# Performance work log

Hardware: AMD Instinct MI355X
Metric: run time of the kernel (lower is better)

## Reference

```python
import jax, jax.numpy as jnp
import numpy as np

N, S = 65536, 2048        # dense points, sampled centres
D1, D2 = 64, 256          # skip-feature dim, centre-embedding dim
MLP = [256, 128]          # conv1x1 channel stack
BN_EPS = 1e-5             # flax BatchNorm default
INTERP_EPS = 1e-8


def setup_inputs() -> dict:
    key = jax.random.key(0)
    ks = jax.random.split(key, 6)
    inp = {
        "xyz1": jax.random.normal(ks[0], (3, N), jnp.float32),
        "xyz2": jax.random.normal(ks[1], (3, S), jnp.float32),
        "points1": jax.random.normal(ks[2], (D1, N), jnp.float32),
        "points2": jax.random.normal(ks[3], (D2, S), jnp.float32),
    }
    c_in = D1 + D2
    for i, c_out in enumerate(MLP):
        inp[f"w{i}"] = jax.random.normal(ks[4 + i], (c_in, c_out), jnp.float32) / np.float32(np.sqrt(c_in))
        inp[f"b{i}"] = jnp.zeros((c_out,), jnp.float32)
        inp[f"scale{i}"] = jnp.ones((c_out,), jnp.float32)
        inp[f"bias{i}"] = jnp.zeros((c_out,), jnp.float32)
        inp[f"mean{i}"] = jnp.zeros((c_out,), jnp.float32)   # BN running mean
        inp[f"var{i}"] = jnp.ones((c_out,), jnp.float32)     # BN running var
        c_in = c_out
    return inp


def reference(xyz1, xyz2, points1, points2,
              w0, b0, scale0, bias0, mean0, var0,
              w1, b1, scale1, bias1, mean1, var1):
    x1 = xyz1.T            # [N, 3]
    x2 = xyz2.T            # [S, 3]
    p2 = points2.T         # [S, D2]

    # squared pairwise distances [N, S]
    dists = (jnp.sum(x1 * x1, -1, keepdims=True)
             + jnp.sum(x2 * x2, -1)[None, :]
             - 2.0 * (x1 @ x2.T))

    # 3 nearest neighbours (smallest dist) per dense point
    neg_d3, idx = jax.lax.top_k(-dists, 3)      # [N, 3]
    d3 = -neg_d3
    recip = 1.0 / (d3 + INTERP_EPS)
    w = recip / jnp.sum(recip, axis=1, keepdims=True)   # [N, 3]

    # inverse-distance-weighted interpolation: [N, D2]
    interp = jnp.einsum('nkd,nk->nd', p2[idx], w)

    new = jnp.concatenate([points1.T, interp], axis=-1)  # [N, D1+D2]

    # conv1x1 (== dense) + BN (inference, running stats) + ReLU stack
    for W, b, s, bb, m, v in ((w0, b0, scale0, bias0, mean0, var0),
                              (w1, b1, scale1, bias1, mean1, var1)):
        y = new @ W + b
        y = (y - m) * (s / jnp.sqrt(v + BN_EPS)) + bb
        new = jax.nn.relu(y)

    return new.T           # [MLP[-1], N]
```

## Files before the change

kernel.cpp:

```cpp
#include <hip/hip_runtime.h>
#include <math.h>

#define NPTS 65536
#define NS   2048
#define C2   256
#define C3   128

#define WS_XYZ2P   0
#define WS_P2T     32768
#define WS_W0F     1081344
#define WS_W1F     1245184
#define WS_AB0     1310720
#define WS_AB1     1312768
#define WS_KIDX    1313792
#define WS_KW      2100224

typedef __attribute__((ext_vector_type(8))) short bf16x8;
typedef __attribute__((ext_vector_type(4))) float f32x4;

__device__ __forceinline__ unsigned short f2bf(float f) {
  unsigned u = __builtin_bit_cast(unsigned, f);
  u = (u + 0x7FFFu + ((u >> 16) & 1u)) >> 16;
  return (unsigned short)u;
}
__device__ __forceinline__ float bf2f(unsigned h) {
  return __builtin_bit_cast(float, h << 16);
}

__global__ __launch_bounds__(256) void pnfp_prep(
    const float* __restrict__ xyz2,
    const float* __restrict__ w0, const float* __restrict__ b0,
    const float* __restrict__ scale0, const float* __restrict__ bias0,
    const float* __restrict__ mean0, const float* __restrict__ var0,
    const float* __restrict__ w1, const float* __restrict__ b1,
    const float* __restrict__ scale1, const float* __restrict__ bias1,
    const float* __restrict__ mean1, const float* __restrict__ var1,
    unsigned char* __restrict__ ws)
{
  int gid = blockIdx.x * 256 + threadIdx.x;

  if (gid < 2048) {
    float x = xyz2[gid], y = xyz2[NS + gid], z = xyz2[2 * NS + gid];
    float sc;
    {
#pragma clang fp contract(off)
      sc = (x * x + y * y) + z * z;
    }
    ((float4*)(ws + WS_XYZ2P))[gid] = make_float4(x, y, z, sc);
    return;
  }
  gid -= 2048;
  if (gid < 81920) {
    int i = gid & 7, l = (gid >> 3) & 63, c = (gid >> 9) & 15, ks = gid >> 13;
    int k = ks * 32 + (l >> 4) * 8 + i;
    int col = c * 16 + (l & 15);
    ((unsigned short*)(ws + WS_W0F))[gid] = f2bf(w0[k * C2 + col]);
    return;
  }
  gid -= 81920;
  if (gid < 32768) {
    int i = gid & 7, l = (gid >> 3) & 63, c = (gid >> 9) & 7, ks = gid >> 12;
    int k = ks * 32 + (l >> 4) * 8 + i;
    int col = c * 16 + (l & 15);
    ((unsigned short*)(ws + WS_W1F))[gid] = f2bf(w1[k * C3 + col]);
    return;
  }
  gid -= 32768;
  if (gid < 256) {
    float a = scale0[gid] / sqrtf(var0[gid] + 1e-5f);
    float bb = (b0[gid] - mean0[gid]) * a + bias0[gid];
    float* ab = (float*)(ws + WS_AB0);
    ab[gid] = a; ab[256 + gid] = bb;
    return;
  }
  gid -= 256;
  if (gid < 128) {
    float a = scale1[gid] / sqrtf(var1[gid] + 1e-5f);
    float bb = (b1[gid] - mean1[gid]) * a + bias1[gid];
    float* ab = (float*)(ws + WS_AB1);
    ab[gid] = a; ab[128 + gid] = bb;
  }
}

__global__ __launch_bounds__(256) void pnfp_tpose(
    const float* __restrict__ points2, unsigned char* __restrict__ ws)
{
  __shared__ float tile[64][65];
  const int st = blockIdx.x & 31;
  const int dt = blockIdx.x >> 5;
  const int tid = threadIdx.x;
#pragma unroll
  for (int it = 0; it < 16; ++it) {
    int j = it * 256 + tid;
    int d = j >> 6, s = j & 63;
    tile[d][s] = points2[(dt * 64 + d) * NS + st * 64 + s];
  }
  __syncthreads();
  unsigned short* p2t = (unsigned short*)(ws + WS_P2T);
#pragma unroll
  for (int it = 0; it < 16; ++it) {
    int j = it * 256 + tid;
    int s = j >> 6, d = j & 63;
    p2t[(st * 64 + s) * 256 + dt * 64 + d] = f2bf(tile[d][s]);
  }
}

__global__ __launch_bounds__(256) void pnfp_knn(
    const float* __restrict__ xyz1, unsigned char* __restrict__ ws)
{
  __shared__ float4 cs[4 * 513];
  const float4* c4 = (const float4*)(ws + WS_XYZ2P);
  for (int j = threadIdx.x; j < NS; j += 256) {
    int qq = j >> 9, tt = j & 511;
    cs[qq * 513 + tt] = c4[j];
  }
  __syncthreads();

  const int tid = threadIdx.x;
  const int q = tid & 3;
  const int n = blockIdx.x * 64 + (tid >> 2);
  const float x = xyz1[n], y = xyz1[NPTS + n], z = xyz1[2 * NPTS + n];
  float sx;
  {
#pragma clang fp contract(off)
    sx = (x * x + y * y) + z * z;
  }
  float d0 = 1e30f, d1 = 1e30f, d2 = 1e30f;
  int i0 = 0, i1 = 0, i2 = 0;
  const float4* cq = cs + q * 513;
  const int sbase = q << 9;
#pragma unroll 8
  for (int t = 0; t < 512; ++t) {
    float4 c = cq[t];
    float dot = fmaf(z, c.z, fmaf(y, c.y, x * c.x));
    float d = (sx + c.w) - 2.0f * dot;
    if (d < d2) {
      const bool lt1 = d < d1, lt0 = d < d0;
      const int s = sbase + t;
      d2 = lt1 ? d1 : d;  i2 = lt1 ? i1 : s;
      d1 = lt0 ? d0 : (lt1 ? d : d1);
      i1 = lt0 ? i0 : (lt1 ? s : i1);
      d0 = lt0 ? d : d0;  i0 = lt0 ? s : i0;
    }
  }
#pragma unroll
  for (int m = 1; m <= 2; m <<= 1) {
    float e0 = __shfl_xor(d0, m), e1 = __shfl_xor(d1, m), e2 = __shfl_xor(d2, m);
    int  j0 = __shfl_xor(i0, m), j1 = __shfl_xor(i1, m), j2 = __shfl_xor(i2, m);
    bool t0 = e0 < d0;
    float r0 = t0 ? e0 : d0; int ri0 = t0 ? j0 : i0;
    float X0 = t0 ? d0 : d1,  X1 = t0 ? d1 : d2;
    int  XI0 = t0 ? i0 : i1, XI1 = t0 ? i1 : i2;
    float Y0 = t0 ? e1 : e0,  Y1v = t0 ? e2 : e1;
    int  YJ0 = t0 ? j1 : j0, YJ1 = t0 ? j2 : j1;
    bool t1 = Y0 < X0;
    float r1 = t1 ? Y0 : X0; int ri1 = t1 ? YJ0 : XI0;
    float X0b = t1 ? X0 : X1; int XI0b = t1 ? XI0 : XI1;
    float Y0b = t1 ? Y1v : Y0; int YJ0b = t1 ? YJ1 : YJ0;
    bool t2 = Y0b < X0b;
    float r2 = t2 ? Y0b : X0b; int ri2 = t2 ? YJ0b : XI0b;
    d0 = r0; d1 = r1; d2 = r2; i0 = ri0; i1 = ri1; i2 = ri2;
  }

  if (q == 0) {
    float q0 = 1.0f / (d0 + 1e-8f);
    float q1 = 1.0f / (d1 + 1e-8f);
    float q2 = 1.0f / (d2 + 1e-8f);
    float qs = (q0 + q1) + q2;
    int* oi = (int*)(ws + WS_KIDX) + 3 * n;
    float* owp = (float*)(ws + WS_KW) + 3 * n;
    oi[0] = i0; oi[1] = i1; oi[2] = i2;
    owp[0] = q0 / qs; owp[1] = q1 / qs; owp[2] = q2 / qs;
  }
}

__global__ __launch_bounds__(256, 3) void pnfp_fused(
    const float* __restrict__ points1,
    const unsigned char* __restrict__ ws,
    float* __restrict__ out)
{
  __shared__ __align__(16) unsigned char smem[41984];
  unsigned short* Fh = (unsigned short*)smem;
  const unsigned short* p2t = (const unsigned short*)(ws + WS_P2T);
  const unsigned short* w0f = (const unsigned short*)(ws + WS_W0F);
  const unsigned short* w1f = (const unsigned short*)(ws + WS_W1F);
  const float* ab0 = (const float*)(ws + WS_AB0);
  const float* ab1 = (const float*)(ws + WS_AB1);
  const int* kidx = (const int*)(ws + WS_KIDX);
  const float* kw = (const float*)(ws + WS_KW);

  const int tid = threadIdx.x;
  const int wv = tid >> 6, lane = tid & 63;
  const int n0 = blockIdx.x * 64;

#pragma unroll
  for (int it = 0; it < 16; ++it) {
    int j = tid + it * 256;
    int d = j >> 6, r = j & 63;
    Fh[r * 328 + d] = f2bf(points1[d * NPTS + n0 + r]);
  }
  {
    const int dbase = lane * 4;
#pragma unroll 2
    for (int rr = 0; rr < 16; ++rr) {
      const int r = wv * 16 + rr, n = n0 + r;
      const int a0 = kidx[3 * n], a1 = kidx[3 * n + 1], a2 = kidx[3 * n + 2];
      const float w0 = kw[3 * n], w1 = kw[3 * n + 1], w2 = kw[3 * n + 2];
      uint2 u0 = *(const uint2*)(p2t + a0 * 256 + dbase);
      uint2 u1 = *(const uint2*)(p2t + a1 * 256 + dbase);
      uint2 u2 = *(const uint2*)(p2t + a2 * 256 + dbase);
      float f0 = fmaf(w2, bf2f(u2.x & 0xFFFFu), fmaf(w1, bf2f(u1.x & 0xFFFFu), w0 * bf2f(u0.x & 0xFFFFu)));
      float f1 = fmaf(w2, bf2f(u2.x >> 16),     fmaf(w1, bf2f(u1.x >> 16),     w0 * bf2f(u0.x >> 16)));
      float f2v = fmaf(w2, bf2f(u2.y & 0xFFFFu), fmaf(w1, bf2f(u1.y & 0xFFFFu), w0 * bf2f(u0.y & 0xFFFFu)));
      float f3 = fmaf(w2, bf2f(u2.y >> 16),     fmaf(w1, bf2f(u1.y >> 16),     w0 * bf2f(u0.y >> 16)));
      uint2 pk;
      pk.x = (unsigned)f2bf(f0) | ((unsigned)f2bf(f1) << 16);
      pk.y = (unsigned)f2bf(f2v) | ((unsigned)f2bf(f3) << 16);
      *(uint2*)(Fh + r * 328 + 64 + dbase) = pk;
    }
  }
  __syncthreads();

  f32x4 zero4 = {0.f, 0.f, 0.f, 0.f};
  f32x4 acc[4][4];
#pragma unroll
  for (int a = 0; a < 4; ++a)
#pragma unroll
    for (int b = 0; b < 4; ++b) acc[a][b] = zero4;

  const int arow = lane & 15;
  const int koff = (lane >> 4) * 8;
  bf16x8 bcur[4], bnxt[4];
#pragma unroll
  for (int ct = 0; ct < 4; ++ct)
    bcur[ct] = *(const bf16x8*)(w0f + ((wv * 4 + ct) * 64 + lane) * 8);
  for (int ks = 0; ks < 10; ++ks) {
#pragma unroll
    for (int ct = 0; ct < 4; ++ct)
      bnxt[ct] = *(const bf16x8*)(w0f + (((ks + 1) * 16 + wv * 4 + ct) * 64 + lane) * 8);
    bf16x8 af[4];
#pragma unroll
    for (int rt = 0; rt < 4; ++rt)
      af[rt] = *(const bf16x8*)(Fh + (rt * 16 + arow) * 328 + ks * 32 + koff);
#pragma unroll
    for (int ct = 0; ct < 4; ++ct)
#pragma unroll
      for (int rt = 0; rt < 4; ++rt)
        acc[rt][ct] = __builtin_amdgcn_mfma_f32_16x16x32_bf16(af[rt], bcur[ct], acc[rt][ct], 0, 0, 0);
#pragma unroll
    for (int ct = 0; ct < 4; ++ct) bcur[ct] = bnxt[ct];
  }
  __syncthreads();

  unsigned short* Y1 = (unsigned short*)smem;
#pragma unroll
  for (int ct = 0; ct < 4; ++ct) {
    const int c = wv * 64 + ct * 16 + arow;
    const float a = ab0[c], b = ab0[256 + c];
#pragma unroll
    for (int rt = 0; rt < 4; ++rt) {
      const int rbase = rt * 16 + (lane >> 4) * 4;
#pragma unroll
      for (int qi = 0; qi < 4; ++qi) {
        float yv = fmaxf(fmaf(acc[rt][ct][qi], a, b), 0.0f);
        Y1[(rbase + qi) * 264 + c] = f2bf(yv);
      }
    }
  }
  __syncthreads();

  f32x4 acc2[4][2];
#pragma unroll
  for (int a = 0; a < 4; ++a) { acc2[a][0] = zero4; acc2[a][1] = zero4; }
  bf16x8 b2cur[2], b2nxt[2];
#pragma unroll
  for (int ct = 0; ct < 2; ++ct)
    b2cur[ct] = *(const bf16x8*)(w1f + ((wv * 2 + ct) * 64 + lane) * 8);
  for (int ks = 0; ks < 8; ++ks) {
#pragma unroll
    for (int ct = 0; ct < 2; ++ct)
      b2nxt[ct] = *(const bf16x8*)(w1f + (((ks + 1) * 8 + wv * 2 + ct) * 64 + lane) * 8);
    bf16x8 af[4];
#pragma unroll
    for (int rt = 0; rt < 4; ++rt)
      af[rt] = *(const bf16x8*)(Y1 + (rt * 16 + arow) * 264 + ks * 32 + koff);
#pragma unroll
    for (int ct = 0; ct < 2; ++ct)
#pragma unroll
      for (int rt = 0; rt < 4; ++rt)
        acc2[rt][ct] = __builtin_amdgcn_mfma_f32_16x16x32_bf16(af[rt], b2cur[ct], acc2[rt][ct], 0, 0, 0);
#pragma unroll
    for (int ct = 0; ct < 2; ++ct) b2cur[ct] = b2nxt[ct];
  }
  __syncthreads();

  float* OUT = (float*)smem;
#pragma unroll
  for (int ct = 0; ct < 2; ++ct) {
    const int c = wv * 32 + ct * 16 + arow;
    const float a = ab1[c], b = ab1[128 + c];
#pragma unroll
    for (int rt = 0; rt < 4; ++rt) {
      const int rbase = rt * 16 + (lane >> 4) * 4;
#pragma unroll
      for (int qi = 0; qi < 4; ++qi)
        OUT[c * 67 + rbase + qi] = fmaxf(fmaf(acc2[rt][ct][qi], a, b), 0.0f);
    }
  }
  __syncthreads();
#pragma unroll
  for (int it = 0; it < 32; ++it) {
    int j = tid + it * 256;
    int c = j >> 6, n = j & 63;
    out[c * NPTS + n0 + n] = OUT[c * 67 + n];
  }
}

extern "C" void kernel_launch(void* const* d_in, const int* in_sizes, int n_in,
                              void* d_out, int out_size, void* d_ws, size_t ws_size,
                              hipStream_t stream) {
  (void)in_sizes; (void)n_in; (void)out_size; (void)ws_size;
  const float* xyz1    = (const float*)d_in[0];
  const float* xyz2    = (const float*)d_in[1];
  const float* points1 = (const float*)d_in[2];
  const float* points2 = (const float*)d_in[3];
  const float* w0      = (const float*)d_in[4];
  const float* b0      = (const float*)d_in[5];
  const float* scale0  = (const float*)d_in[6];
  const float* bias0   = (const float*)d_in[7];
  const float* mean0   = (const float*)d_in[8];
  const float* var0    = (const float*)d_in[9];
  const float* w1      = (const float*)d_in[10];
  const float* b1      = (const float*)d_in[11];
  const float* scale1  = (const float*)d_in[12];
  const float* bias1   = (const float*)d_in[13];
  const float* mean1   = (const float*)d_in[14];
  const float* var1    = (const float*)d_in[15];
  unsigned char* ws = (unsigned char*)d_ws;
  float* out = (float*)d_out;

  pnfp_prep<<<458, 256, 0, stream>>>(xyz2, w0, b0, scale0, bias0, mean0, var0,
                                     w1, b1, scale1, bias1, mean1, var1, ws);
  pnfp_tpose<<<128, 256, 0, stream>>>(points2, ws);
  pnfp_knn<<<1024, 256, 0, stream>>>(xyz1, ws);
  pnfp_fused<<<1024, 256, 0, stream>>>(points1, ws, out);
}
```

Baseline: 190.1 us.

## Register-block KNN over four points per thread and merge transpose into prep

The KNN kernel now has each thread handle four dense points against a 256-centre slice, so each shared-memory centre load is reused four times. The branchy top-3 insertion is replaced with branchless med3/min updates, and the 8-way partial results are merged with a shuffle reduction. Centre norms are computed inside the KNN kernel, and the points2 transpose is folded into the prep kernel, which removes one launch. In exchange the kernel uses more registers and the always-executed update costs more ALU work per candidate.

```diff
diff --git a/kernel.cpp b/kernel.cpp
--- a/kernel.cpp
+++ b/kernel.cpp
@@ -28,7 +28,7 @@
 }
 
 __global__ __launch_bounds__(256) void pnfp_prep(
-    const float* __restrict__ xyz2,
+    const float* __restrict__ points2,
     const float* __restrict__ w0, const float* __restrict__ b0,
     const float* __restrict__ scale0, const float* __restrict__ bias0,
     const float* __restrict__ mean0, const float* __restrict__ var0,
@@ -37,19 +37,30 @@
     const float* __restrict__ mean1, const float* __restrict__ var1,
     unsigned char* __restrict__ ws)
 {
-  int gid = blockIdx.x * 256 + threadIdx.x;
-
-  if (gid < 2048) {
-    float x = xyz2[gid], y = xyz2[NS + gid], z = xyz2[2 * NS + gid];
-    float sc;
-    {
-#pragma clang fp contract(off)
-      sc = (x * x + y * y) + z * z;
-    }
-    ((float4*)(ws + WS_XYZ2P))[gid] = make_float4(x, y, z, sc);
+  __shared__ float tile[64][65];
+  const int tid = threadIdx.x;
+
+  if (blockIdx.x < 128) {
+    const int st = blockIdx.x & 31;
+    const int dt = blockIdx.x >> 5;
+#pragma unroll
+    for (int it = 0; it < 16; ++it) {
+      int j = it * 256 + tid;
+      int d = j >> 6, s = j & 63;
+      tile[d][s] = points2[(dt * 64 + d) * NS + st * 64 + s];
+    }
+    __syncthreads();
+    unsigned short* p2t = (unsigned short*)(ws + WS_P2T);
+#pragma unroll
+    for (int it = 0; it < 16; ++it) {
+      int j = it * 256 + tid;
+      int s = j >> 6, d = j & 63;
+      p2t[(st * 64 + s) * 256 + dt * 64 + d] = f2bf(tile[d][s]);
+    }
     return;
   }
-  gid -= 2048;
+
+  int gid = (blockIdx.x - 128) * 256 + tid;
   if (gid < 81920) {
     int i = gid & 7, l = (gid >> 3) & 63, c = (gid >> 9) & 15, ks = gid >> 13;
     int k = ks * 32 + (l >> 4) * 8 + i;
@@ -82,95 +93,102 @@
   }
 }
 
-__global__ __launch_bounds__(256) void pnfp_tpose(
-    const float* __restrict__ points2, unsigned char* __restrict__ ws)
+__global__ __launch_bounds__(256) void pnfp_knn(
+    const float* __restrict__ xyz1, const float* __restrict__ xyz2,
+    unsigned char* __restrict__ ws)
 {
-  __shared__ float tile[64][65];
-  const int st = blockIdx.x & 31;
-  const int dt = blockIdx.x >> 5;
+  __shared__ float4 cs[2056];
+  for (int j = threadIdx.x; j < NS; j += 256) {
+    float x = xyz2[j], y = xyz2[NS + j], z = xyz2[2 * NS + j];
+    float sc;
+    {
+#pragma clang fp contract(off)
+      sc = (x * x + y * y) + z * z;
+    }
+    cs[j + (j >> 8)] = make_float4(x, y, z, sc);
+  }
+  __syncthreads();
+
   const int tid = threadIdx.x;
-#pragma unroll
-  for (int it = 0; it < 16; ++it) {
-    int j = it * 256 + tid;
-    int d = j >> 6, s = j & 63;
-    tile[d][s] = points2[(dt * 64 + d) * NS + st * 64 + s];
-  }
-  __syncthreads();
-  unsigned short* p2t = (unsigned short*)(ws + WS_P2T);
-#pragma unroll
-  for (int it = 0; it < 16; ++it) {
-    int j = it * 256 + tid;
-    int s = j >> 6, d = j & 63;
-    p2t[(st * 64 + s) * 256 + dt * 64 + d] = f2bf(tile[d][s]);
-  }
-}
-
-__global__ __launch_bounds__(256) void pnfp_knn(
-    const float* __restrict__ xyz1, unsigned char* __restrict__ ws)
-{
-  __shared__ float4 cs[4 * 513];
-  const float4* c4 = (const float4*)(ws + WS_XYZ2P);
-  for (int j = threadIdx.x; j < NS; j += 256) {
-    int qq = j >> 9, tt = j & 511;
-    cs[qq * 513 + tt] = c4[j];
-  }
-  __syncthreads();
-
-  const int tid = threadIdx.x;
-  const int q = tid & 3;
-  const int n = blockIdx.x * 64 + (tid >> 2);
-  const float x = xyz1[n], y = xyz1[NPTS + n], z = xyz1[2 * NPTS + n];
-  float sx;
-  {
+  const int rank = tid & 7;
+  const int set = tid >> 3;
+  const int nb = blockIdx.x * 128 + set * 4;
+
+  float px[4], py[4], pz[4], ps[4];
+#pragma unroll
+  for (int p = 0; p < 4; ++p) {
+    int n = nb + p;
+    px[p] = xyz1[n]; py[p] = xyz1[NPTS + n]; pz[p] = xyz1[2 * NPTS + n];
+    {
 #pragma clang fp contract(off)
-    sx = (x * x + y * y) + z * z;
-  }
-  float d0 = 1e30f, d1 = 1e30f, d2 = 1e30f;
-  int i0 = 0, i1 = 0, i2 = 0;
-  const float4* cq = cs + q * 513;
-  const int sbase = q << 9;
-#pragma unroll 8
-  for (int t = 0; t < 512; ++t) {
-    float4 c = cq[t];
-    float dot = fmaf(z, c.z, fmaf(y, c.y, x * c.x));
-    float d = (sx + c.w) - 2.0f * dot;
-    if (d < d2) {
-      const bool lt1 = d < d1, lt0 = d < d0;
-      const int s = sbase + t;
-      d2 = lt1 ? d1 : d;  i2 = lt1 ? i1 : s;
-      d1 = lt0 ? d0 : (lt1 ? d : d1);
-      i1 = lt0 ? i0 : (lt1 ? s : i1);
-      d0 = lt0 ? d : d0;  i0 = lt0 ? s : i0;
-    }
-  }
-#pragma unroll
-  for (int m = 1; m <= 2; m <<= 1) {
-    float e0 = __shfl_xor(d0, m), e1 = __shfl_xor(d1, m), e2 = __shfl_xor(d2, m);
-    int  j0 = __shfl_xor(i0, m), j1 = __shfl_xor(i1, m), j2 = __shfl_xor(i2, m);
-    bool t0 = e0 < d0;
-    float r0 = t0 ? e0 : d0; int ri0 = t0 ? j0 : i0;
-    float X0 = t0 ? d0 : d1,  X1 = t0 ? d1 : d2;
-    int  XI0 = t0 ? i0 : i1, XI1 = t0 ? i1 : i2;
-    float Y0 = t0 ? e1 : e0,  Y1v = t0 ? e2 : e1;
-    int  YJ0 = t0 ? j1 : j0, YJ1 = t0 ? j2 : j1;
-    bool t1 = Y0 < X0;
-    float r1 = t1 ? Y0 : X0; int ri1 = t1 ? YJ0 : XI0;
-    float X0b = t1 ? X0 : X1; int XI0b = t1 ? XI0 : XI1;
-    float Y0b = t1 ? Y1v : Y0; int YJ0b = t1 ? YJ1 : YJ0;
-    bool t2 = Y0b < X0b;
-    float r2 = t2 ? Y0b : X0b; int ri2 = t2 ? YJ0b : XI0b;
-    d0 = r0; d1 = r1; d2 = r2; i0 = ri0; i1 = ri1; i2 = ri2;
-  }
-
-  if (q == 0) {
-    float q0 = 1.0f / (d0 + 1e-8f);
-    float q1 = 1.0f / (d1 + 1e-8f);
-    float q2 = 1.0f / (d2 + 1e-8f);
-    float qs = (q0 + q1) + q2;
-    int* oi = (int*)(ws + WS_KIDX) + 3 * n;
-    float* owp = (float*)(ws + WS_KW) + 3 * n;
-    oi[0] = i0; oi[1] = i1; oi[2] = i2;
-    owp[0] = q0 / qs; owp[1] = q1 / qs; owp[2] = q2 / qs;
+      ps[p] = (px[p] * px[p] + py[p] * py[p]) + pz[p] * pz[p];
+    }
+  }
+
+  float D0[4], D1[4], D2[4];
+  int I0[4], I1[4], I2[4];
+#pragma unroll
+  for (int p = 0; p < 4; ++p) {
+    D0[p] = 1e30f; D1[p] = 1e30f; D2[p] = 1e30f;
+    I0[p] = 0; I1[p] = 0; I2[p] = 0;
+  }
+
+  const float4* cq = cs + rank * 257;
+  const int sbase = rank << 8;
+#pragma unroll 4
+  for (int t = 0; t < 256; ++t) {
+    const float4 c = cq[t];
+    const int s = sbase + t;
+#pragma unroll
+    for (int p = 0; p < 4; ++p) {
+      float dot = fmaf(pz[p], c.z, fmaf(py[p], c.y, px[p] * c.x));
+      float d = (ps[p] + c.w) - 2.0f * dot;
+      const bool c2 = d < D2[p], c1 = d < D1[p], c0 = d < D0[p];
+      I2[p] = c2 ? (c1 ? I1[p] : s) : I2[p];
+      I1[p] = c1 ? (c0 ? I0[p] : s) : I1[p];
+      I0[p] = c0 ? s : I0[p];
+      float n1 = __builtin_amdgcn_fmed3f(D0[p], D1[p], d);
+      float n2 = __builtin_amdgcn_fmed3f(D1[p], D2[p], d);
+      D0[p] = fminf(D0[p], d);
+      D1[p] = n1; D2[p] = n2;
+    }
+  }
+
+#pragma unroll
+  for (int p = 0; p < 4; ++p) {
+#pragma unroll
+    for (int m = 1; m <= 4; m <<= 1) {
+      float e0 = __shfl_xor(D0[p], m), e1 = __shfl_xor(D1[p], m), e2 = __shfl_xor(D2[p], m);
+      int  j0 = __shfl_xor(I0[p], m), j1 = __shfl_xor(I1[p], m), j2 = __shfl_xor(I2[p], m);
+      bool t0 = e0 < D0[p];
+      float r0 = t0 ? e0 : D0[p]; int ri0 = t0 ? j0 : I0[p];
+      float X0 = t0 ? D0[p] : D1[p], X1 = t0 ? D1[p] : D2[p];
+      int  XI0 = t0 ? I0[p] : I1[p], XI1 = t0 ? I1[p] : I2[p];
+      float Y0 = t0 ? e1 : e0, Y1v = t0 ? e2 : e1;
+      int  YJ0 = t0 ? j1 : j0, YJ1 = t0 ? j2 : j1;
+      bool t1 = Y0 < X0;
+      float r1 = t1 ? Y0 : X0; int ri1 = t1 ? YJ0 : XI0;
+      float X0b = t1 ? X0 : X1; int XI0b = t1 ? XI0 : XI1;
+      float Y0b = t1 ? Y1v : Y0; int YJ0b = t1 ? YJ1 : YJ0;
+      bool t2 = Y0b < X0b;
+      float r2 = t2 ? Y0b : X0b; int ri2 = t2 ? YJ0b : XI0b;
+      D0[p] = r0; D1[p] = r1; D2[p] = r2; I0[p] = ri0; I1[p] = ri1; I2[p] = ri2;
+    }
+  }
+
+  if (rank == 0) {
+#pragma unroll
+    for (int p = 0; p < 4; ++p) {
+      const int n = nb + p;
+      float q0 = 1.0f / (D0[p] + 1e-8f);
+      float q1 = 1.0f / (D1[p] + 1e-8f);
+      float q2 = 1.0f / (D2[p] + 1e-8f);
+      float qs = (q0 + q1) + q2;
+      int* oi = (int*)(ws + WS_KIDX) + 3 * n;
+      float* owp = (float*)(ws + WS_KW) + 3 * n;
+      oi[0] = I0[p]; oi[1] = I1[p]; oi[2] = I2[p];
+      owp[0] = q0 / qs; owp[1] = q1 / qs; owp[2] = q2 / qs;
+    }
   }
 }
 
@@ -339,9 +357,8 @@
   unsigned char* ws = (unsigned char*)d_ws;
   float* out = (float*)d_out;
 
-  pnfp_prep<<<458, 256, 0, stream>>>(xyz2, w0, b0, scale0, bias0, mean0, var0,
+  pnfp_prep<<<578, 256, 0, stream>>>(points2, w0, b0, scale0, bias0, mean0, var0,
                                      w1, b1, scale1, bias1, mean1, var1, ws);
-  pnfp_tpose<<<128, 256, 0, stream>>>(points2, ws);
-  pnfp_knn<<<1024, 256, 0, stream>>>(xyz1, ws);
+  pnfp_knn<<<512, 256, 0, stream>>>(xyz1, xyz2, ws);
   pnfp_fused<<<1024, 256, 0, stream>>>(points1, ws, out);
 }
```

Result: slower. 206.5 us (+8.6%).
